# Optimization experiments

Hardware: AMD Instinct MI355X
Metric: run time of the kernel (lower is better)

The kernel has to match this reference:

```python
import jax, jax.numpy as jnp
import numpy as np

B, T, F, H = 2048, 16, 768, 1024  # batch(nodes), timesteps, 3*input_size, hidden_size


def setup_inputs() -> dict:
    key = jax.random.key(0)
    k1, k2, k3 = jax.random.split(key, 3)
    s_ih = 1.0 / np.sqrt(F)
    s_hh = 1.0 / np.sqrt(H)
    return {
        "x": jax.random.normal(k1, (B, T, F), dtype=jnp.float32),
        "W_ih": jax.random.normal(k2, (F, 4 * H), dtype=jnp.float32) * s_ih,
        "W_hh": jax.random.normal(k3, (H, 4 * H), dtype=jnp.float32) * s_hh,
        "b": jnp.zeros((4 * H,), dtype=jnp.float32),
    }


def reference(x, W_ih, W_hh, b):
    # Batched equivalent of the original per-sample python loop:
    # each sample's [T, F] sequence runs through the LSTM; the final hidden
    # state [H] per sample is concatenated and reshaped to (-1, B).
    Bb, Tt, Ff = x.shape
    Hh = W_hh.shape[0]
    x_t = jnp.swapaxes(x, 0, 1)  # [T, B, F]

    def step(carry, xt):
        h, c = carry
        gates = xt @ W_ih + h @ W_hh + b  # [B, 4H]
        i, f, g, o = jnp.split(gates, 4, axis=-1)
        c = jax.nn.sigmoid(f) * c + jax.nn.sigmoid(i) * jnp.tanh(g)
        h = jax.nn.sigmoid(o) * jnp.tanh(c)
        return (h, c), None

    h0 = jnp.zeros((Bb, Hh), dtype=x.dtype)
    (h, _), _ = jax.lax.scan(step, (h0, h0), x_t)
    # torch.cat over batch of [H] vectors -> flat [B*H], then reshape(-1, B)
    return h.reshape(-1).reshape(-1, Bb)
```

## Files before the change

### kernel.cpp

```cpp
#include <hip/hip_runtime.h>
#include <hip/hip_bf16.h>
#include <stdint.h>

#define B_  2048
#define T_  16
#define F_  768
#define H_  1024
#define G4_ 4096

typedef __attribute__((ext_vector_type(8))) __bf16 bf16x8;
typedef __attribute__((ext_vector_type(4))) float  f32x4;

static __device__ __forceinline__ unsigned short f2bf(float f) {
    union { float f; uint32_t u; } v; v.f = f;
    uint32_t u = v.u;
    uint32_t r = (u + 0x7fffu + ((u >> 16) & 1u)) >> 16;
    return (unsigned short)r;
}
static __device__ __forceinline__ unsigned short f2h(float f) {
    union { _Float16 h; unsigned short u; } v; v.h = (_Float16)f; return v.u;
}
static __device__ __forceinline__ float h2f(unsigned short u) {
    union { _Float16 h; unsigned short u; } v; v.u = u; return (float)v.h;
}
static __device__ __forceinline__ float sigf(float x) {
    return 1.0f / (1.0f + __expf(-x));
}
static __device__ __forceinline__ float tanhfast(float x) {
    return 2.0f / (1.0f + __expf(-2.0f * x)) - 1.0f;
}

#define GLOAD_LDS16(gsrc, ldst)                                                       \
    __builtin_amdgcn_global_load_lds((const __attribute__((address_space(1))) void*)(gsrc), \
                                     (__attribute__((address_space(3))) void*)(ldst), \
                                     16, 0, 0)


__global__ void prep_kernel(const float* __restrict__ x, unsigned short* __restrict__ xbf,
                            const float* __restrict__ Wih, unsigned short* __restrict__ wih_t,
                            const float* __restrict__ Whh, unsigned short* __restrict__ whh_t) {
    const int bid = blockIdx.x;
    const int tid = threadIdx.x;
    if (bid < 24576) {
        int idx = bid * 256 + tid;
        float4 v = *(const float4*)(x + (size_t)idx * 4);
        ushort4 o;
        o.x = f2bf(v.x); o.y = f2bf(v.y); o.z = f2bf(v.z); o.w = f2bf(v.w);
        *(ushort4*)(xbf + (size_t)idx * 4) = o;
        return;
    }
    __shared__ float tile[32][33];
    const float* w;
    unsigned short* wt;
    int K, mode, idx;
    if (bid < 24576 + 3072) { w = Wih; wt = wih_t; K = F_; mode = 0; idx = bid - 24576; }
    else                    { w = Whh; wt = whh_t; K = H_; mode = 1; idx = bid - 27648; }
    int nb = (idx & 127) * 32;
    int kb = (idx >> 7) * 32;
    int tx = tid & 31, ty = tid >> 5;
    #pragma unroll
    for (int i = 0; i < 32; i += 8)
        tile[ty + i][tx] = w[(size_t)(kb + ty + i) * G4_ + nb + tx];
    __syncthreads();
    #pragma unroll
    for (int i = 0; i < 32; i += 8) {
        int n = nb + ty + i;
        int g = n >> 10;
        int j = n & 1023;
        int np = mode ? ((j >> 4) * 64 + g * 16 + (j & 15))
                      : ((j >> 6) * 256 + g * 64 + ((j >> 4) & 3) * 16 + (j & 15));
        wt[(size_t)np * K + kb + tx] = f2bf(tile[tx][ty + i]);
    }
}


#define STAGE4(bufi, kind, half, gbase, ld, rowbase, kt) do {                         \
    const int kel_ = (kt) * 64;                                                       \
    _Pragma("unroll")                                                                 \
    for (int r2 = 0; r2 < 2; ++r2) {                                                  \
        const int rih_ = r2 * 64 + (tid >> 3);                                        \
        const int ch_  = (tid & 7) ^ (rih_ & 7);                                      \
        GLOAD_LDS16((gbase) + (size_t)((rowbase) + (half) * 128 + rih_) * (ld)        \
                            + kel_ + ch_ * 8,                                         \
                    &lds[bufi][kind][half][r2 * 4096 + tid * 8]);                     \
    }                                                                                 \
} while (0)

#define RD4_A(half_, mb)                                                              \
    _Pragma("unroll")                                                                 \
    for (int mm = 0; mm < 4; ++mm) {                                                  \
        const int row_ = ((mb) + mm) * 32 + wm * 16 + fr;                             \
        _Pragma("unroll")                                                             \
        for (int kk = 0; kk < 2; ++kk)                                                \
            Afr[mm][kk] = *(const bf16x8*)&lds[buf][0][half_]                         \
                [(row_ & 127) * 64 + (((kk * 4 + fq) ^ (row_ & 7)) * 8)];             \
    }

#define RD4_B(half_, nb)                                                              \
    _Pragma("unroll")                                                                 \
    for (int nn = 0; nn < 2; ++nn) {                                                  \
        const int row_ = ((nb) + nn) * 64 + wn * 16 + fr;                             \
        _Pragma("unroll")                                                             \
        for (int kk = 0; kk < 2; ++kk)                                                \
            Bfr[(nb) + nn][kk] = *(const bf16x8*)&lds[buf][1][half_]                  \
                [(row_ & 127) * 64 + (((kk * 4 + fq) ^ (row_ & 7)) * 8)];             \
    }

#define MFMAQ(mb, nb)                                                                 \
    __builtin_amdgcn_s_setprio(1);                                                    \
    _Pragma("unroll")                                                                 \
    for (int mm = 0; mm < 4; ++mm)                                                    \
        _Pragma("unroll")                                                             \
        for (int nn = 0; nn < 2; ++nn)                                                \
            _Pragma("unroll")                                                         \
            for (int kk = 0; kk < 2; ++kk)                                            \
                acc[(mb) + mm][(nb) + nn] = __builtin_amdgcn_mfma_f32_16x16x32_bf16(  \
                    Afr[mm][kk], Bfr[(nb) + nn][kk], acc[(mb) + mm][(nb) + nn], 0, 0, 0); \
    __builtin_amdgcn_s_setprio(0);

#define WAITV4  asm volatile("s_waitcnt vmcnt(10)" ::: "memory");                     \
                __builtin_amdgcn_sched_barrier(0);
#define BARR4   __builtin_amdgcn_s_barrier();                                         \
                __builtin_amdgcn_sched_barrier(0);

#define KLOOP4(ABASE, ALD, BBASE, BLD, NT)                                            \
    STAGE4(0, 0, 0, ABASE, ALD, bm0, 0);                                              \
    STAGE4(0, 1, 0, BBASE, BLD, bn0, 0);                                              \
    STAGE4(0, 1, 1, BBASE, BLD, bn0, 0);                                              \
    STAGE4(0, 0, 1, ABASE, ALD, bm0, 0);                                              \
    STAGE4(1, 0, 0, ABASE, ALD, bm0, 1);                                              \
    STAGE4(1, 1, 0, BBASE, BLD, bn0, 1);                                              \
    STAGE4(1, 1, 1, BBASE, BLD, bn0, 1);                                              \
    WAITV4; BARR4;                                                                    \
    for (int kt = 0; kt < (NT); ++kt) {                                               \
        const int buf = kt & 1, nbuf = buf ^ 1;                                       \
        const int k1 = (kt + 1 < (NT)) ? kt + 1 : (NT) - 1;                           \
        const int k2 = (kt + 2 < (NT)) ? kt + 2 : (NT) - 1;                           \
        bf16x8 Afr[4][2]; bf16x8 Bfr[4][2];                                           \
                                                                             \
        RD4_A(0, 0); RD4_B(0, 0);                                                     \
        STAGE4(nbuf, 0, 1, ABASE, ALD, bm0, k1);                                      \
        WAITV4; BARR4;                                                                \
        MFMAQ(0, 0); BARR4;                                                           \
                                                                             \
        RD4_B(1, 2);                                                                  \
        STAGE4(buf, 0, 0, ABASE, ALD, bm0, k2);                                       \
        WAITV4; BARR4;                                                                \
        MFMAQ(0, 2); BARR4;                                                           \
                                                                             \
        RD4_A(1, 4);                                                                  \
        STAGE4(buf, 1, 0, BBASE, BLD, bn0, k2);                                       \
        BARR4;                                                                        \
        MFMAQ(4, 0); BARR4;                                                           \
                                                                             \
        STAGE4(buf, 1, 1, BBASE, BLD, bn0, k2);                                       \
        WAITV4; BARR4;                                                                \
        MFMAQ(4, 2); BARR4;                                                           \
    }

__global__ __launch_bounds__(512, 2) void xgemm8f_kernel(
        const unsigned short* __restrict__ xbf,
        const unsigned short* __restrict__ wih_t,
        unsigned short* __restrict__ gx,
        const float* __restrict__ bias,
        float* __restrict__ c,
        unsigned short* __restrict__ hbf0) {
    __shared__ __align__(16) unsigned short lds[2][2][2][8192];

    const int bid = blockIdx.x;
    const int xcd = bid & 7;
    const int i   = bid >> 3;
    const int bmg = i >> 6;
    const int r   = i & 63;
    const int bn  = r >> 2;
    const int bm  = xcd * 16 + bmg * 4 + (r & 3);
    const int bm0 = bm * 256, bn0 = bn * 256;

    const int tid = threadIdx.x;
    const int wid = tid >> 6, lane = tid & 63;
    const int wm = wid >> 2, wn = wid & 3;
    const int fr = lane & 15, fq = lane >> 4;

    f32x4 acc[8][4] = {};

    KLOOP4(xbf, F_, wih_t, F_, 12)

    const int j = bn * 64 + wn * 16 + fr;
    float bi_ = 0.f, bg_ = 0.f, bo_ = 0.f;
    if (fq == 0) {
        bi_ = bias[j]; bg_ = bias[2 * H_ + j]; bo_ = bias[3 * H_ + j];
    }
    #pragma unroll
    for (int mm = 0; mm < 8; ++mm) {
        #pragma unroll
        for (int rr = 0; rr < 4; ++rr) {
            int row = bm0 + mm * 32 + wm * 16 + fq * 4 + rr;
            int tt = row & 15, bb = row >> 4;
            ushort4 o;
            o.x = f2h(acc[mm][0][rr]);
            o.y = f2h(acc[mm][1][rr]);
            o.z = f2h(acc[mm][2][rr]);
            o.w = f2h(acc[mm][3][rr]);
            if (tt != 0) {
                *(ushort4*)(gx + (((size_t)tt * B_ + bb) * H_ + j) * 4) = o;
            } else {
                float gi = bi_ + h2f(o.x);
                float gg = bg_ + h2f(o.z);
                float go = bo_ + h2f(o.w);
                float cn = sigf(gi) * tanhfast(gg);
                float hv = sigf(go) * tanhfast(cn);
                size_t off = (size_t)bb * H_ + j;
                c[off] = cn;
                hbf0[off] = f2bf(hv);
            }
        }
    }
}


#define STA6(slot, kt) do {                                                           \
    const int kel_ = (kt) * 64;                                                       \
    _Pragma("unroll")                                                                 \
    for (int r2 = 0; r2 < 2; ++r2) {                                                  \
        const int rih_ = r2 * 32 + (tid >> 3);                                        \
        const int ch_  = (tid & 7) ^ (rih_ & 7);                                      \
        GLOAD_LDS16(hprev + (size_t)(bm0 + rih_) * H_ + kel_ + ch_ * 8,               \
                    &ldsA[slot][r2 * 2048 + tid * 8]);                                \
    }                                                                                 \
} while (0)

#define STB6(slot, rowbase, kt) do {                                                  \
    const int kel_ = (kt) * 64;                                                       \
    _Pragma("unroll")                                                                 \
    for (int r4 = 0; r4 < 4; ++r4) {                                                  \
        const int rih_ = r4 * 32 + (tid >> 3);                                        \
        const int ch_  = (tid & 7) ^ (rih_ & 7);                                      \
        GLOAD_LDS16(whh_t + (size_t)((rowbase) + rih_) * H_ + kel_ + ch_ * 8,         \
                    &ldsB[slot][r4 * 2048 + tid * 8]);                                \
    }                                                                                 \
} while (0)

#define RD_A6(slot, AR)                                                               \
    _Pragma("unroll")                                                                 \
    for (int mm = 0; mm < 2; ++mm) {                                                  \
        const int row_ = wm * 32 + mm * 16 + fr;                                      \
        _Pragma("unroll")                                                             \
        for (int kk = 0; kk < 2; ++kk)                                                \
            AR[mm][kk] = *(const bf16x8*)&ldsA[slot]                                  \
                [row_ * 64 + (((kk * 4 + fq) ^ (row_ & 7)) * 8)];                     \
    }

#define RD_B6(slot, BF)                                                               \
    _Pragma("unroll")                                                                 \
    for (int nf = 0; nf < 4; ++nf) {                                                  \
        const int rowb_ = wn * 64 + nf * 16 + fr;                                     \
        _Pragma("unroll")                                                             \
        for (int kk = 0; kk < 2; ++kk)                                                \
            BF[nf][kk] = *(const bf16x8*)&ldsB[slot]                                  \
                [rowb_ * 64 + (((kk * 4 + fq) ^ (rowb_ & 7)) * 8)];                   \
    }

#define MFMA16S(AR, BF)                                                               \
    __builtin_amdgcn_s_setprio(1);                                                    \
    _Pragma("unroll")                                                                 \
    for (int mm = 0; mm < 2; ++mm)                                                    \
        _Pragma("unroll")                                                             \
        for (int nf = 0; nf < 4; ++nf)                                                \
            _Pragma("unroll")                                                         \
            for (int kk = 0; kk < 2; ++kk)                                            \
                acc[mm][nf] = __builtin_amdgcn_mfma_f32_16x16x32_bf16(                \
                    AR[mm][kk], BF[nf][kk], acc[mm][nf], 0, 0, 0);                    \
    __builtin_amdgcn_s_setprio(0);

#define LGKM0 asm volatile("s_waitcnt lgkmcnt(0)" ::: "memory");
#define BARR  __builtin_amdgcn_s_barrier();

__global__ __launch_bounds__(256, 2) void lstm_step_dp_kernel(
        const unsigned short* __restrict__ hprev,
        const unsigned short* __restrict__ whh_t,
        const unsigned short* __restrict__ gx,
        const float* __restrict__ bias,
        float* __restrict__ c,
        unsigned short* __restrict__ hnext,
        float* __restrict__ hout,
        int t, int last) {
    __shared__ __align__(16) unsigned short ldsA[3][4096];
    __shared__ __align__(16) unsigned short ldsB[3][8192];

    const int bid = blockIdx.x;
    const int xcd = bid & 7;
    const int i   = bid >> 3;
    const int pair = i & 1;
    const int bm  = i >> 1;
    const int bn_base = xcd * 4 + pair * 2;
    const int bm0 = bm * 64;

    const int tid = threadIdx.x;
    const int wid = tid >> 6, lane = tid & 63;
    const int wm = wid >> 1, wn = wid & 1;
    const int fr = lane & 15, fq = lane >> 4;

    const int j0 = (bn_base * 2 + wn) * 16 + fr;
    const int j1 = ((bn_base + 1) * 2 + wn) * 16 + fr;
    const float bi0 = bias[j0], bf0 = bias[H_ + j0], bg0 = bias[2 * H_ + j0], bo0 = bias[3 * H_ + j0];
    const float bi1 = bias[j1], bf1 = bias[H_ + j1], bg1 = bias[2 * H_ + j1], bo1 = bias[3 * H_ + j1];

    f32x4 acc[2][4] = {};
    ushort4 gpre[2][4];
    float   cpre[2][4];

    STA6(0, 0); STB6(0, bn_base * 128, 0);
    STA6(1, 1); STB6(1, bn_base * 128, 1);
    asm volatile("s_waitcnt vmcnt(6)" ::: "memory");
    BARR;

    for (int kt = 0; kt < 32; ++kt) {
        const int s_  = kt % 3;
        const int s2_ = (kt + 2) % 3;
        const int k2  = (kt + 2 < 32) ? kt + 2 : 31;
        const int ak2 = k2 & 15;
        const int brb2 = (bn_base + (k2 >> 4)) * 128;
        bf16x8 Am[2][2], Bf[4][2];
        RD_A6(s_, Am);
        RD_B6(s_, Bf);
        STA6(s2_, ak2);
        STB6(s2_, brb2, ak2);
        if (kt == 13 || kt == 29) {
            const int p_ = kt >> 4;
            const int jp_ = p_ ? j1 : j0;
            #pragma unroll
            for (int mm = 0; mm < 2; ++mm)
                #pragma unroll
                for (int rr = 0; rr < 4; ++rr) {
                    int row_ = bm0 + wm * 32 + mm * 16 + fq * 4 + rr;
                    gpre[mm][rr] = *(const ushort4*)(gx + (((size_t)t * B_ + row_) * H_ + jp_) * 4);
                    cpre[mm][rr] = c[(size_t)row_ * H_ + jp_];
                }
        }
        LGKM0;
        MFMA16S(Am, Bf);
        if (kt == 13 || kt == 14 || kt == 29 || kt == 30)
            asm volatile("s_waitcnt vmcnt(22)" ::: "memory");
        else
            asm volatile("s_waitcnt vmcnt(6)" ::: "memory");
        BARR;
        if (kt == 15) {
            #pragma unroll
            for (int mm = 0; mm < 2; ++mm) {
                #pragma unroll
                for (int rr = 0; rr < 4; ++rr) {
                    int row_ = bm0 + wm * 32 + mm * 16 + fq * 4 + rr;
                    ushort4 g4 = gpre[mm][rr];
                    float gi = acc[mm][0][rr] + bi0 + h2f(g4.x);
                    float gf = acc[mm][1][rr] + bf0 + h2f(g4.y);
                    float gg = acc[mm][2][rr] + bg0 + h2f(g4.z);
                    float go = acc[mm][3][rr] + bo0 + h2f(g4.w);
                    float cn = sigf(gf) * cpre[mm][rr] + sigf(gi) * tanhfast(gg);
                    float hv = sigf(go) * tanhfast(cn);
                    size_t off = (size_t)row_ * H_ + j0;
                    c[off] = cn;
                    hnext[off] = f2bf(hv);
                    if (last) hout[off] = hv;
                }
            }
            #pragma unroll
            for (int mm = 0; mm < 2; ++mm)
                #pragma unroll
                for (int nf = 0; nf < 4; ++nf)
                    #pragma unroll
                    for (int q = 0; q < 4; ++q) acc[mm][nf][q] = 0.0f;
        }
    }

    #pragma unroll
    for (int mm = 0; mm < 2; ++mm) {
        #pragma unroll
        for (int rr = 0; rr < 4; ++rr) {
            int row_ = bm0 + wm * 32 + mm * 16 + fq * 4 + rr;
            ushort4 g4 = gpre[mm][rr];
            float gi = acc[mm][0][rr] + bi1 + h2f(g4.x);
            float gf = acc[mm][1][rr] + bf1 + h2f(g4.y);
            float gg = acc[mm][2][rr] + bg1 + h2f(g4.z);
            float go = acc[mm][3][rr] + bo1 + h2f(g4.w);
            float cn = sigf(gf) * cpre[mm][rr] + sigf(gi) * tanhfast(gg);
            float hv = sigf(go) * tanhfast(cn);
            size_t off = (size_t)row_ * H_ + j1;
            c[off] = cn;
            hnext[off] = f2bf(hv);
            if (last) hout[off] = hv;
        }
    }
}


extern "C" void kernel_launch(void* const* d_in, const int* in_sizes, int n_in,
                              void* d_out, int out_size, void* d_ws, size_t ws_size,
                              hipStream_t stream) {
    const float* x    = (const float*)d_in[0];
    const float* Wih  = (const float*)d_in[1];
    const float* Whh  = (const float*)d_in[2];
    const float* bias = (const float*)d_in[3];
    float* out = (float*)d_out;

    char* ws = (char*)d_ws;
    unsigned short* xbf   = (unsigned short*)(ws);
    unsigned short* wih_t = (unsigned short*)(ws + 50331648);
    unsigned short* whh_t = (unsigned short*)(ws + 56623104);
    unsigned short* hbf0  = (unsigned short*)(ws + 65011712);
    unsigned short* hbf1  = (unsigned short*)(ws + 69206016);
    float*          c     = (float*)(ws + 73400320);
    unsigned short* gx    = (unsigned short*)(ws + 81788928);

    hipLaunchKernelGGL(prep_kernel, dim3(24576 + 3072 + 4096), dim3(256), 0, stream,
                       x, xbf, Wih, wih_t, Whh, whh_t);

    hipLaunchKernelGGL(xgemm8f_kernel, dim3(2048), dim3(512), 0, stream,
                       xbf, wih_t, gx, bias, c, hbf0);

    for (int t = 1; t < T_; ++t) {
        unsigned short* hr = (t & 1) ? hbf0 : hbf1;
        unsigned short* hw = (t & 1) ? hbf1 : hbf0;
        hipLaunchKernelGGL(lstm_step_dp_kernel, dim3(512), dim3(256), 0, stream,
                           hr, whh_t, gx, bias, c, hw, out, t, (t == T_ - 1) ? 1 : 0);
    }
}
```

Baseline: 736.9 us.

## Interleave per-timestep input GEMM slices with recurrent LSTM step kernels

```diff
diff --git a/kernel.cpp b/kernel.cpp
--- a/kernel.cpp
+++ b/kernel.cpp
@@ -7,6 +7,7 @@
 #define F_  768
 #define H_  1024
 #define G4_ 4096
+#define TF_ (T_ * F_)
 
 typedef __attribute__((ext_vector_type(8))) __bf16 bf16x8;
 typedef __attribute__((ext_vector_type(4))) float  f32x4;
@@ -52,9 +53,9 @@
     __shared__ float tile[32][33];
     const float* w;
     unsigned short* wt;
-    int K, mode, idx;
-    if (bid < 24576 + 3072) { w = Wih; wt = wih_t; K = F_; mode = 0; idx = bid - 24576; }
-    else                    { w = Whh; wt = whh_t; K = H_; mode = 1; idx = bid - 27648; }
+    int K, idx;
+    if (bid < 24576 + 3072) { w = Wih; wt = wih_t; K = F_; idx = bid - 24576; }
+    else                    { w = Whh; wt = whh_t; K = H_; idx = bid - 27648; }
     int nb = (idx & 127) * 32;
     int kb = (idx >> 7) * 32;
     int tx = tid & 31, ty = tid >> 5;
@@ -67,175 +68,30 @@
         int n = nb + ty + i;
         int g = n >> 10;
         int j = n & 1023;
-        int np = mode ? ((j >> 4) * 64 + g * 16 + (j & 15))
-                      : ((j >> 6) * 256 + g * 64 + ((j >> 4) & 3) * 16 + (j & 15));
+        int np = (j >> 4) * 64 + g * 16 + (j & 15);
         wt[(size_t)np * K + kb + tx] = f2bf(tile[tx][ty + i]);
     }
 }
 
 
-#define STAGE4(bufi, kind, half, gbase, ld, rowbase, kt) do {                         \
-    const int kel_ = (kt) * 64;                                                       \
-    _Pragma("unroll")                                                                 \
-    for (int r2 = 0; r2 < 2; ++r2) {                                                  \
-        const int rih_ = r2 * 64 + (tid >> 3);                                        \
-        const int ch_  = (tid & 7) ^ (rih_ & 7);                                      \
-        GLOAD_LDS16((gbase) + (size_t)((rowbase) + (half) * 128 + rih_) * (ld)        \
-                            + kel_ + ch_ * 8,                                         \
-                    &lds[bufi][kind][half][r2 * 4096 + tid * 8]);                     \
-    }                                                                                 \
-} while (0)
-
-#define RD4_A(half_, mb)                                                              \
-    _Pragma("unroll")                                                                 \
-    for (int mm = 0; mm < 4; ++mm) {                                                  \
-        const int row_ = ((mb) + mm) * 32 + wm * 16 + fr;                             \
-        _Pragma("unroll")                                                             \
-        for (int kk = 0; kk < 2; ++kk)                                                \
-            Afr[mm][kk] = *(const bf16x8*)&lds[buf][0][half_]                         \
-                [(row_ & 127) * 64 + (((kk * 4 + fq) ^ (row_ & 7)) * 8)];             \
-    }
-
-#define RD4_B(half_, nb)                                                              \
-    _Pragma("unroll")                                                                 \
-    for (int nn = 0; nn < 2; ++nn) {                                                  \
-        const int row_ = ((nb) + nn) * 64 + wn * 16 + fr;                             \
-        _Pragma("unroll")                                                             \
-        for (int kk = 0; kk < 2; ++kk)                                                \
-            Bfr[(nb) + nn][kk] = *(const bf16x8*)&lds[buf][1][half_]                  \
-                [(row_ & 127) * 64 + (((kk * 4 + fq) ^ (row_ & 7)) * 8)];             \
-    }
-
-#define MFMAQ(mb, nb)                                                                 \
-    __builtin_amdgcn_s_setprio(1);                                                    \
-    _Pragma("unroll")                                                                 \
-    for (int mm = 0; mm < 4; ++mm)                                                    \
-        _Pragma("unroll")                                                             \
-        for (int nn = 0; nn < 2; ++nn)                                                \
-            _Pragma("unroll")                                                         \
-            for (int kk = 0; kk < 2; ++kk)                                            \
-                acc[(mb) + mm][(nb) + nn] = __builtin_amdgcn_mfma_f32_16x16x32_bf16(  \
-                    Afr[mm][kk], Bfr[(nb) + nn][kk], acc[(mb) + mm][(nb) + nn], 0, 0, 0); \
-    __builtin_amdgcn_s_setprio(0);
-
-#define WAITV4  asm volatile("s_waitcnt vmcnt(10)" ::: "memory");                     \
-                __builtin_amdgcn_sched_barrier(0);
-#define BARR4   __builtin_amdgcn_s_barrier();                                         \
-                __builtin_amdgcn_sched_barrier(0);
-
-#define KLOOP4(ABASE, ALD, BBASE, BLD, NT)                                            \
-    STAGE4(0, 0, 0, ABASE, ALD, bm0, 0);                                              \
-    STAGE4(0, 1, 0, BBASE, BLD, bn0, 0);                                              \
-    STAGE4(0, 1, 1, BBASE, BLD, bn0, 0);                                              \
-    STAGE4(0, 0, 1, ABASE, ALD, bm0, 0);                                              \
-    STAGE4(1, 0, 0, ABASE, ALD, bm0, 1);                                              \
-    STAGE4(1, 1, 0, BBASE, BLD, bn0, 1);                                              \
-    STAGE4(1, 1, 1, BBASE, BLD, bn0, 1);                                              \
-    WAITV4; BARR4;                                                                    \
-    for (int kt = 0; kt < (NT); ++kt) {                                               \
-        const int buf = kt & 1, nbuf = buf ^ 1;                                       \
-        const int k1 = (kt + 1 < (NT)) ? kt + 1 : (NT) - 1;                           \
-        const int k2 = (kt + 2 < (NT)) ? kt + 2 : (NT) - 1;                           \
-        bf16x8 Afr[4][2]; bf16x8 Bfr[4][2];                                           \
-                                                                             \
-        RD4_A(0, 0); RD4_B(0, 0);                                                     \
-        STAGE4(nbuf, 0, 1, ABASE, ALD, bm0, k1);                                      \
-        WAITV4; BARR4;                                                                \
-        MFMAQ(0, 0); BARR4;                                                           \
-                                                                             \
-        RD4_B(1, 2);                                                                  \
-        STAGE4(buf, 0, 0, ABASE, ALD, bm0, k2);                                       \
-        WAITV4; BARR4;                                                                \
-        MFMAQ(0, 2); BARR4;                                                           \
-                                                                             \
-        RD4_A(1, 4);                                                                  \
-        STAGE4(buf, 1, 0, BBASE, BLD, bn0, k2);                                       \
-        BARR4;                                                                        \
-        MFMAQ(4, 0); BARR4;                                                           \
-                                                                             \
-        STAGE4(buf, 1, 1, BBASE, BLD, bn0, k2);                                       \
-        WAITV4; BARR4;                                                                \
-        MFMAQ(4, 2); BARR4;                                                           \
-    }
-
-__global__ __launch_bounds__(512, 2) void xgemm8f_kernel(
-        const unsigned short* __restrict__ xbf,
-        const unsigned short* __restrict__ wih_t,
-        unsigned short* __restrict__ gx,
-        const float* __restrict__ bias,
-        float* __restrict__ c,
-        unsigned short* __restrict__ hbf0) {
-    __shared__ __align__(16) unsigned short lds[2][2][2][8192];
-
-    const int bid = blockIdx.x;
-    const int xcd = bid & 7;
-    const int i   = bid >> 3;
-    const int bmg = i >> 6;
-    const int r   = i & 63;
-    const int bn  = r >> 2;
-    const int bm  = xcd * 16 + bmg * 4 + (r & 3);
-    const int bm0 = bm * 256, bn0 = bn * 256;
-
-    const int tid = threadIdx.x;
-    const int wid = tid >> 6, lane = tid & 63;
-    const int wm = wid >> 2, wn = wid & 3;
-    const int fr = lane & 15, fq = lane >> 4;
-
-    f32x4 acc[8][4] = {};
-
-    KLOOP4(xbf, F_, wih_t, F_, 12)
-
-    const int j = bn * 64 + wn * 16 + fr;
-    float bi_ = 0.f, bg_ = 0.f, bo_ = 0.f;
-    if (fq == 0) {
-        bi_ = bias[j]; bg_ = bias[2 * H_ + j]; bo_ = bias[3 * H_ + j];
-    }
-    #pragma unroll
-    for (int mm = 0; mm < 8; ++mm) {
-        #pragma unroll
-        for (int rr = 0; rr < 4; ++rr) {
-            int row = bm0 + mm * 32 + wm * 16 + fq * 4 + rr;
-            int tt = row & 15, bb = row >> 4;
-            ushort4 o;
-            o.x = f2h(acc[mm][0][rr]);
-            o.y = f2h(acc[mm][1][rr]);
-            o.z = f2h(acc[mm][2][rr]);
-            o.w = f2h(acc[mm][3][rr]);
-            if (tt != 0) {
-                *(ushort4*)(gx + (((size_t)tt * B_ + bb) * H_ + j) * 4) = o;
-            } else {
-                float gi = bi_ + h2f(o.x);
-                float gg = bg_ + h2f(o.z);
-                float go = bo_ + h2f(o.w);
-                float cn = sigf(gi) * tanhfast(gg);
-                float hv = sigf(go) * tanhfast(cn);
-                size_t off = (size_t)bb * H_ + j;
-                c[off] = cn;
-                hbf0[off] = f2bf(hv);
-            }
-        }
-    }
-}
-
-
-#define STA6(slot, kt) do {                                                           \
+#define STG_A(slot, srcp, ld, base, kt) do {                                          \
     const int kel_ = (kt) * 64;                                                       \
     _Pragma("unroll")                                                                 \
     for (int r2 = 0; r2 < 2; ++r2) {                                                  \
         const int rih_ = r2 * 32 + (tid >> 3);                                        \
         const int ch_  = (tid & 7) ^ (rih_ & 7);                                      \
-        GLOAD_LDS16(hprev + (size_t)(bm0 + rih_) * H_ + kel_ + ch_ * 8,               \
+        GLOAD_LDS16((srcp) + (size_t)((base) + rih_) * (ld) + kel_ + ch_ * 8,         \
                     &ldsA[slot][r2 * 2048 + tid * 8]);                                \
     }                                                                                 \
 } while (0)
 
-#define STB6(slot, rowbase, kt) do {                                                  \
+#define STG_B(slot, srcp, ld, base, kt) do {                                          \
     const int kel_ = (kt) * 64;                                                       \
     _Pragma("unroll")                                                                 \
     for (int r4 = 0; r4 < 4; ++r4) {                                                  \
         const int rih_ = r4 * 32 + (tid >> 3);                                        \
         const int ch_  = (tid & 7) ^ (rih_ & 7);                                      \
-        GLOAD_LDS16(whh_t + (size_t)((rowbase) + rih_) * H_ + kel_ + ch_ * 8,         \
+        GLOAD_LDS16((srcp) + (size_t)((base) + rih_) * (ld) + kel_ + ch_ * 8,         \
                     &ldsB[slot][r4 * 2048 + tid * 8]);                                \
     }                                                                                 \
 } while (0)
@@ -273,121 +129,234 @@
     __builtin_amdgcn_s_setprio(0);
 
 #define LGKM0 asm volatile("s_waitcnt lgkmcnt(0)" ::: "memory");
+#define WAIT6 asm volatile("s_waitcnt vmcnt(6)" ::: "memory");
 #define BARR  __builtin_amdgcn_s_barrier();
 
-__global__ __launch_bounds__(256, 2) void lstm_step_dp_kernel(
+#define XGEMM_BODY(tslice, bm0x, bn0x)                                                \
+    const unsigned short* srcax = xbf + (size_t)(tslice) * F_;                        \
+    STG_A(0, srcax, TF_, bm0x, 0); STG_B(0, wih_t, F_, bn0x, 0);                      \
+    STG_A(1, srcax, TF_, bm0x, 1); STG_B(1, wih_t, F_, bn0x, 1);                      \
+    WAIT6; BARR;                                                                      \
+    for (int kt = 0; kt < 12; ++kt) {                                                 \
+        const int s_ = kt % 3, s2_ = (kt + 2) % 3;                                    \
+        const int k2_ = (kt + 2 < 12) ? kt + 2 : 11;                                  \
+        bf16x8 Am[2][2], Bf[4][2];                                                    \
+        RD_A6(s_, Am); RD_B6(s_, Bf);                                                 \
+        STG_A(s2_, srcax, TF_, bm0x, k2_);                                            \
+        STG_B(s2_, wih_t, F_, bn0x, k2_);                                             \
+        LGKM0;                                                                        \
+        MFMA16S(Am, Bf);                                                              \
+        WAIT6; BARR;                                                                  \
+    }
+
+
+__global__ __launch_bounds__(256, 2) void xslice_kernel(
+        const unsigned short* __restrict__ xbf,
+        const unsigned short* __restrict__ wih_t,
+        unsigned short* __restrict__ gx,
+        const float* __restrict__ bias,
+        float* __restrict__ c,
+        unsigned short* __restrict__ hbf0) {
+    __shared__ __align__(16) unsigned short ldsA[3][4096];
+    __shared__ __align__(16) unsigned short ldsB[3][8192];
+
+    const int tid = threadIdx.x;
+    const int wid = tid >> 6, lane = tid & 63;
+    const int wm = wid >> 1, wn = wid & 1;
+    const int fr = lane & 15, fq = lane >> 4;
+
+    const int bid = blockIdx.x;
+    const int t01 = bid >> 10;
+    const int xid = bid & 1023;
+    const int xcd = xid & 7;
+    const int ii  = xid >> 3;
+    const int bnx = xcd * 4 + (ii & 3);
+    const int bmx = ii >> 2;
+    const int bm0x = bmx * 64, bn0x = bnx * 128;
+
+    f32x4 acc[2][4] = {};
+    XGEMM_BODY(t01, bm0x, bn0x)
+
+    const int j = (bnx * 2 + wn) * 16 + fr;
+    if (t01 == 1) {
+        #pragma unroll
+        for (int mm = 0; mm < 2; ++mm) {
+            #pragma unroll
+            for (int rr = 0; rr < 4; ++rr) {
+                int row = bm0x + wm * 32 + mm * 16 + fq * 4 + rr;
+                ushort4 o;
+                o.x = f2h(acc[mm][0][rr]);
+                o.y = f2h(acc[mm][1][rr]);
+                o.z = f2h(acc[mm][2][rr]);
+                o.w = f2h(acc[mm][3][rr]);
+                *(ushort4*)(gx + (((size_t)1 * B_ + row) * H_ + j) * 4) = o;
+            }
+        }
+    } else {
+        const float bi = bias[j], bg = bias[2 * H_ + j], bo = bias[3 * H_ + j];
+        #pragma unroll
+        for (int mm = 0; mm < 2; ++mm) {
+            #pragma unroll
+            for (int rr = 0; rr < 4; ++rr) {
+                int row = bm0x + wm * 32 + mm * 16 + fq * 4 + rr;
+                float gi = bi + h2f(f2h(acc[mm][0][rr]));
+                float gg = bg + h2f(f2h(acc[mm][2][rr]));
+                float go = bo + h2f(f2h(acc[mm][3][rr]));
+                float cn = sigf(gi) * tanhfast(gg);
+                float hv = sigf(go) * tanhfast(cn);
+                size_t off = (size_t)row * H_ + j;
+                c[off] = cn;
+                hbf0[off] = f2bf(hv);
+            }
+        }
+    }
+}
+
+
+__global__ __launch_bounds__(256, 2) void lstm_fused_kernel(
         const unsigned short* __restrict__ hprev,
         const unsigned short* __restrict__ whh_t,
-        const unsigned short* __restrict__ gx,
+        const unsigned short* __restrict__ xbf,
+        const unsigned short* __restrict__ wih_t,
+        unsigned short* __restrict__ gx,
         const float* __restrict__ bias,
         float* __restrict__ c,
         unsigned short* __restrict__ hnext,
         float* __restrict__ hout,
-        int t, int last) {
+        int t, int last, int has_x) {
     __shared__ __align__(16) unsigned short ldsA[3][4096];
     __shared__ __align__(16) unsigned short ldsB[3][8192];
-
-    const int bid = blockIdx.x;
-    const int xcd = bid & 7;
-    const int i   = bid >> 3;
-    const int pair = i & 1;
-    const int bm  = i >> 1;
-    const int bn_base = xcd * 4 + pair * 2;
-    const int bm0 = bm * 64;
 
     const int tid = threadIdx.x;
     const int wid = tid >> 6, lane = tid & 63;
     const int wm = wid >> 1, wn = wid & 1;
     const int fr = lane & 15, fq = lane >> 4;
 
-    const int j0 = (bn_base * 2 + wn) * 16 + fr;
-    const int j1 = ((bn_base + 1) * 2 + wn) * 16 + fr;
-    const float bi0 = bias[j0], bf0 = bias[H_ + j0], bg0 = bias[2 * H_ + j0], bo0 = bias[3 * H_ + j0];
-    const float bi1 = bias[j1], bf1 = bias[H_ + j1], bg1 = bias[2 * H_ + j1], bo1 = bias[3 * H_ + j1];
-
-    f32x4 acc[2][4] = {};
-    ushort4 gpre[2][4];
-    float   cpre[2][4];
-
-    STA6(0, 0); STB6(0, bn_base * 128, 0);
-    STA6(1, 1); STB6(1, bn_base * 128, 1);
-    asm volatile("s_waitcnt vmcnt(6)" ::: "memory");
-    BARR;
-
-    for (int kt = 0; kt < 32; ++kt) {
-        const int s_  = kt % 3;
-        const int s2_ = (kt + 2) % 3;
-        const int k2  = (kt + 2 < 32) ? kt + 2 : 31;
-        const int ak2 = k2 & 15;
-        const int brb2 = (bn_base + (k2 >> 4)) * 128;
-        bf16x8 Am[2][2], Bf[4][2];
-        RD_A6(s_, Am);
-        RD_B6(s_, Bf);
-        STA6(s2_, ak2);
-        STB6(s2_, brb2, ak2);
-        if (kt == 13 || kt == 29) {
-            const int p_ = kt >> 4;
-            const int jp_ = p_ ? j1 : j0;
+    const int bid = blockIdx.x;
+    int sid = bid, is_step = 1;
+    if (has_x) { is_step = ((bid % 3) == 0); sid = bid / 3; }
+
+    if (is_step) {
+        const int xcd = sid & 7;
+        const int i   = sid >> 3;
+        const int pair = i & 1;
+        const int bm  = i >> 1;
+        const int bn_base = xcd * 4 + pair * 2;
+        const int bm0 = bm * 64;
+
+        const int j0 = (bn_base * 2 + wn) * 16 + fr;
+        const int j1 = ((bn_base + 1) * 2 + wn) * 16 + fr;
+        const float bi0 = bias[j0], bf0 = bias[H_ + j0], bg0 = bias[2 * H_ + j0], bo0 = bias[3 * H_ + j0];
+        const float bi1 = bias[j1], bf1 = bias[H_ + j1], bg1 = bias[2 * H_ + j1], bo1 = bias[3 * H_ + j1];
+
+        f32x4 acc[2][4] = {};
+        ushort4 gpre[2][4];
+        float   cpre[2][4];
+
+        STG_A(0, hprev, H_, bm0, 0); STG_B(0, whh_t, H_, bn_base * 128, 0);
+        STG_A(1, hprev, H_, bm0, 1); STG_B(1, whh_t, H_, bn_base * 128, 1);
+        WAIT6; BARR;
+
+        for (int kt = 0; kt < 32; ++kt) {
+            const int s_  = kt % 3;
+            const int s2_ = (kt + 2) % 3;
+            const int k2  = (kt + 2 < 32) ? kt + 2 : 31;
+            const int ak2 = k2 & 15;
+            const int brb2 = (bn_base + (k2 >> 4)) * 128;
+            bf16x8 Am[2][2], Bf[4][2];
+            RD_A6(s_, Am);
+            RD_B6(s_, Bf);
+            STG_A(s2_, hprev, H_, bm0, ak2);
+            STG_B(s2_, whh_t, H_, brb2, ak2);
+            if (kt == 13 || kt == 29) {
+                const int p_ = kt >> 4;
+                const int jp_ = p_ ? j1 : j0;
+                #pragma unroll
+                for (int mm = 0; mm < 2; ++mm)
+                    #pragma unroll
+                    for (int rr = 0; rr < 4; ++rr) {
+                        int row_ = bm0 + wm * 32 + mm * 16 + fq * 4 + rr;
+                        gpre[mm][rr] = *(const ushort4*)(gx + (((size_t)t * B_ + row_) * H_ + jp_) * 4);
+                        cpre[mm][rr] = c[(size_t)row_ * H_ + jp_];
+                    }
+            }
+            LGKM0;
+            MFMA16S(Am, Bf);
+            if (kt == 13 || kt == 14 || kt == 29 || kt == 30)
+                asm volatile("s_waitcnt vmcnt(22)" ::: "memory");
+            else
+                asm volatile("s_waitcnt vmcnt(6)" ::: "memory");
+            BARR;
+            if (kt == 15) {
+                #pragma unroll
+                for (int mm = 0; mm < 2; ++mm) {
+                    #pragma unroll
+                    for (int rr = 0; rr < 4; ++rr) {
+                        int row_ = bm0 + wm * 32 + mm * 16 + fq * 4 + rr;
+                        ushort4 g4 = gpre[mm][rr];
+                        float gi = acc[mm][0][rr] + bi0 + h2f(g4.x);
+                        float gf = acc[mm][1][rr] + bf0 + h2f(g4.y);
+                        float gg = acc[mm][2][rr] + bg0 + h2f(g4.z);
+                        float go = acc[mm][3][rr] + bo0 + h2f(g4.w);
+                        float cn = sigf(gf) * cpre[mm][rr] + sigf(gi) * tanhfast(gg);
+                        float hv = sigf(go) * tanhfast(cn);
+                        size_t off = (size_t)row_ * H_ + j0;
+                        c[off] = cn;
+                        hnext[off] = f2bf(hv);
+                        if (last) hout[off] = hv;
+                    }
+                }
+                #pragma unroll
+                for (int mm = 0; mm < 2; ++mm)
+                    #pragma unroll
+                    for (int nf = 0; nf < 4; ++nf)
+                        #pragma unroll
+                        for (int q = 0; q < 4; ++q) acc[mm][nf][q] = 0.0f;
+            }
+        }
+
+        #pragma unroll
+        for (int mm = 0; mm < 2; ++mm) {
             #pragma unroll
-            for (int mm = 0; mm < 2; ++mm)
-                #pragma unroll
-                for (int rr = 0; rr < 4; ++rr) {
-                    int row_ = bm0 + wm * 32 + mm * 16 + fq * 4 + rr;
-                    gpre[mm][rr] = *(const ushort4*)(gx + (((size_t)t * B_ + row_) * H_ + jp_) * 4);
-                    cpre[mm][rr] = c[(size_t)row_ * H_ + jp_];
-                }
-        }
-        LGKM0;
-        MFMA16S(Am, Bf);
-        if (kt == 13 || kt == 14 || kt == 29 || kt == 30)
-            asm volatile("s_waitcnt vmcnt(22)" ::: "memory");
-        else
-            asm volatile("s_waitcnt vmcnt(6)" ::: "memory");
-        BARR;
-        if (kt == 15) {
+            for (int rr = 0; rr < 4; ++rr) {
+                int row_ = bm0 + wm * 32 + mm * 16 + fq * 4 + rr;
+                ushort4 g4 = gpre[mm][rr];
+                float gi = acc[mm][0][rr] + bi1 + h2f(g4.x);
+                float gf = acc[mm][1][rr] + bf1 + h2f(g4.y);
+                float gg = acc[mm][2][rr] + bg1 + h2f(g4.z);
+                float go = acc[mm][3][rr] + bo1 + h2f(g4.w);
+                float cn = sigf(gf) * cpre[mm][rr] + sigf(gi) * tanhfast(gg);
+                float hv = sigf(go) * tanhfast(cn);
+                size_t off = (size_t)row_ * H_ + j1;
+                c[off] = cn;
+                hnext[off] = f2bf(hv);
+                if (last) hout[off] = hv;
+            }
+        }
+    } else {
+        const int xid = bid - bid / 3 - 1;
+        const int xcd = xid & 7;
+        const int ii  = xid >> 3;
+        const int bnx = xcd * 4 + (ii & 3);
+        const int bmx = ii >> 2;
+        const int bm0x = bmx * 64, bn0x = bnx * 128;
+
+        f32x4 acc[2][4] = {};
+        XGEMM_BODY(t + 1, bm0x, bn0x)
+
+        const int j = (bnx * 2 + wn) * 16 + fr;
+        #pragma unroll
+        for (int mm = 0; mm < 2; ++mm) {
             #pragma unroll
-            for (int mm = 0; mm < 2; ++mm) {
-                #pragma unroll
-                for (int rr = 0; rr < 4; ++rr) {
-                    int row_ = bm0 + wm * 32 + mm * 16 + fq * 4 + rr;
-                    ushort4 g4 = gpre[mm][rr];
-                    float gi = acc[mm][0][rr] + bi0 + h2f(g4.x);
-                    float gf = acc[mm][1][rr] + bf0 + h2f(g4.y);
-                    float gg = acc[mm][2][rr] + bg0 + h2f(g4.z);
-                    float go = acc[mm][3][rr] + bo0 + h2f(g4.w);
-                    float cn = sigf(gf) * cpre[mm][rr] + sigf(gi) * tanhfast(gg);
-                    float hv = sigf(go) * tanhfast(cn);
-                    size_t off = (size_t)row_ * H_ + j0;
-                    c[off] = cn;
-                    hnext[off] = f2bf(hv);
-                    if (last) hout[off] = hv;
-                }
-            }
-            #pragma unroll
-            for (int mm = 0; mm < 2; ++mm)
-                #pragma unroll
-                for (int nf = 0; nf < 4; ++nf)
-                    #pragma unroll
-                    for (int q = 0; q < 4; ++q) acc[mm][nf][q] = 0.0f;
-        }
-    }
-
-    #pragma unroll
-    for (int mm = 0; mm < 2; ++mm) {
-        #pragma unroll
-        for (int rr = 0; rr < 4; ++rr) {
-            int row_ = bm0 + wm * 32 + mm * 16 + fq * 4 + rr;
-            ushort4 g4 = gpre[mm][rr];
-            float gi = acc[mm][0][rr] + bi1 + h2f(g4.x);
-            float gf = acc[mm][1][rr] + bf1 + h2f(g4.y);
-            float gg = acc[mm][2][rr] + bg1 + h2f(g4.z);
-            float go = acc[mm][3][rr] + bo1 + h2f(g4.w);
-            float cn = sigf(gf) * cpre[mm][rr] + sigf(gi) * tanhfast(gg);
-            float hv = sigf(go) * tanhfast(cn);
-            size_t off = (size_t)row_ * H_ + j1;
-            c[off] = cn;
-            hnext[off] = f2bf(hv);
-            if (last) hout[off] = hv;
+            for (int rr = 0; rr < 4; ++rr) {
+                int row = bm0x + wm * 32 + mm * 16 + fq * 4 + rr;
+                ushort4 o;
+                o.x = f2h(acc[mm][0][rr]);
+                o.y = f2h(acc[mm][1][rr]);
+                o.z = f2h(acc[mm][2][rr]);
+                o.w = f2h(acc[mm][3][rr]);
+                *(ushort4*)(gx + (((size_t)(t + 1) * B_ + row) * H_ + j) * 4) = o;
+            }
         }
     }
 }
@@ -414,13 +383,16 @@
     hipLaunchKernelGGL(prep_kernel, dim3(24576 + 3072 + 4096), dim3(256), 0, stream,
                        x, xbf, Wih, wih_t, Whh, whh_t);
 
-    hipLaunchKernelGGL(xgemm8f_kernel, dim3(2048), dim3(512), 0, stream,
+    hipLaunchKernelGGL(xslice_kernel, dim3(2048), dim3(256), 0, stream,
                        xbf, wih_t, gx, bias, c, hbf0);
 
     for (int t = 1; t < T_; ++t) {
         unsigned short* hr = (t & 1) ? hbf0 : hbf1;
         unsigned short* hw = (t & 1) ? hbf1 : hbf0;
-        hipLaunchKernelGGL(lstm_step_dp_kernel, dim3(512), dim3(256), 0, stream,
-                           hr, whh_t, gx, bias, c, hw, out, t, (t == T_ - 1) ? 1 : 0);
-    }
-}
+        int has_x = (t < T_ - 1) ? 1 : 0;
+        int grid  = has_x ? 1536 : 512;
+        hipLaunchKernelGGL(lstm_fused_kernel, dim3(grid), dim3(256), 0, stream,
+                           hr, whh_t, xbf, wih_t, gx, bias, c, hw, out,
+                           t, (t == T_ - 1) ? 1 : 0, has_x);
+    }
+}
```

Result: slower. 1.005 ms (+36.3%).
